# Optimization experiments

Hardware: AMD Instinct MI355X
Metric: run time of the kernel (lower is better)

## Reference

```python
import jax, jax.numpy as jnp
import numpy as np

N, M, E, HID, H = 50000, 4000, 320000, 128, 2
EPS = 1e-5  # torch BatchNorm1d eps


def _lrelu(x):
    return jnp.where(x >= 0, x, 0.2 * x)


def _bn(x, g, b):
    # BatchNorm1d in training mode: biased batch statistics over dim 0
    m = x.mean(0)
    v = ((x - m) ** 2).mean(0)
    return g * (x - m) * jax.lax.rsqrt(v + EPS) + b


def _seg_softmax(a, idx, n):
    # softmax of a[E,heads] normalized per node index idx (PyG softmax)
    mx = jax.ops.segment_max(a, idx, num_segments=n)
    e = jnp.exp(a - mx[idx])
    s = jax.ops.segment_sum(e, idx, num_segments=n)
    return e / s[idx]


def _hgconv(x, he_n, he_e, he_w, W, att, bias, heads):
    # PyG HypergraphConv(use_attention=True, concat=False)
    xl = (x @ W).reshape(N, heads, HID)                  # lin(x) -> [N,heads,C]
    # hyperedge_attr = incidence^T @ x  (matches to_dense_adj path in HGAT)
    ea = jax.ops.segment_sum(x[he_n], he_e, num_segments=M)  # [M,F]
    eal = (ea @ W).reshape(M, heads, HID)                # lin(hyperedge_attr)
    a = (jnp.concatenate([xl[he_n], eal[he_e]], axis=-1) * att[0]).sum(-1)  # [E,heads]
    a = _seg_softmax(_lrelu(a), he_n, N)
    # degree normalizations
    Dn = jax.ops.segment_sum(he_w[he_e], he_n, num_segments=N)
    Dinv = jnp.where(Dn > 0, 1.0 / Dn, 0.0)
    Bn = jax.ops.segment_sum(jnp.ones((E,), x.dtype), he_e, num_segments=M)
    Binv = jnp.where(Bn > 0, 1.0 / Bn, 0.0)
    # node -> hyperedge
    m1 = Binv[he_e][:, None, None] * xl[he_n] * a[..., None]
    eo = jax.ops.segment_sum(m1, he_e, num_segments=M)   # [M,heads,C]
    # hyperedge -> node
    m2 = Dinv[he_n][:, None, None] * eo[he_e] * a[..., None]
    out = jax.ops.segment_sum(m2, he_n, num_segments=N)  # [N,heads,C]
    return out.mean(1) + bias                            # concat=False -> head mean


def _forward(x, he_w, lin1_w, lin1_b, bn1_g, bn1_b, h1_w, h1_att, h1_b,
             bn2_g, bn2_b, h2_w, h2_att, h2_b, bn3_g, bn3_b,
             lin2_w, lin2_b, bn4_g, bn4_b, he_n, he_e):
    src = x
    x = _bn(_lrelu(x @ lin1_w + lin1_b), bn1_g, bn1_b)
    x2 = _hgconv(x, he_n, he_e, he_w, h1_w, h1_att, h1_b, H)
    x = _bn(x + x2, bn2_g, bn2_b)
    x2 = _hgconv(x, he_n, he_e, he_w, h2_w, h2_att, h2_b, 1)
    x = _bn(x + x2, bn3_g, bn3_b)
    x = _lrelu(x @ lin2_w + lin2_b)
    return _bn(src + x, bn4_g, bn4_b)


def setup_inputs() -> dict:
    key = jax.random.key(0)
    ks = jax.random.split(key, 10)
    s = 0.05
    he_n = jax.random.randint(ks[0], (E,), 0, N, dtype=jnp.int32)
    he_e = (jnp.arange(E, dtype=jnp.int32) % M)  # every hyperedge id used
    return {
        'x': jax.random.normal(ks[1], (N, 128), jnp.float32),
        'he_n': he_n, 'he_e': he_e,
        'he_w': jnp.ones((M,), jnp.float32),
        'lin1_w': jax.random.normal(ks[2], (128, HID), jnp.float32) * s,
        'lin1_b': jnp.zeros((HID,), jnp.float32),
        'bn1_g': jnp.ones((HID,), jnp.float32), 'bn1_b': jnp.zeros((HID,), jnp.float32),
        'h1_w': jax.random.normal(ks[3], (HID, H * HID), jnp.float32) * s,
        'h1_att': jax.random.normal(ks[4], (1, H, 2 * HID), jnp.float32) * s,
        'h1_b': jnp.zeros((HID,), jnp.float32),
        'bn2_g': jnp.ones((HID,), jnp.float32), 'bn2_b': jnp.zeros((HID,), jnp.float32),
        'h2_w': jax.random.normal(ks[5], (HID, HID), jnp.float32) * s,
        'h2_att': jax.random.normal(ks[6], (1, 1, 2 * HID), jnp.float32) * s,
        'h2_b': jnp.zeros((HID,), jnp.float32),
        'bn3_g': jnp.ones((HID,), jnp.float32), 'bn3_b': jnp.zeros((HID,), jnp.float32),
        'lin2_w': jax.random.normal(ks[7], (HID, 128), jnp.float32) * s,
        'lin2_b': jnp.zeros((128,), jnp.float32),
        'bn4_g': jnp.ones((128,), jnp.float32), 'bn4_b': jnp.zeros((128,), jnp.float32),
    }


def reference(x, he_n, he_e, he_w, lin1_w, lin1_b, bn1_g, bn1_b, h1_w, h1_att, h1_b,
              bn2_g, bn2_b, h2_w, h2_att, h2_b, bn3_g, bn3_b,
              lin2_w, lin2_b, bn4_g, bn4_b):
    return _forward(x, he_w, lin1_w, lin1_b, bn1_g, bn1_b, h1_w, h1_att, h1_b,
                    bn2_g, bn2_b, h2_w, h2_att, h2_b, bn3_g, bn3_b,
                    lin2_w, lin2_b, bn4_g, bn4_b, he_n, he_e)
```

## Files before the change

kernel.cpp:

```cpp
#include <hip/hip_runtime.h>
#include <math.h>

constexpr int Nn = 50000;
constexpr int Mm = 4000;
constexpr int Ee = 320000;
constexpr int KPB = Ee / Mm;
constexpr float BINV = 1.0f / (float)KPB;
constexpr float EPSf = 1e-5f;
constexpr int NBKT = 16;
constexpr int NBSCAN = 49;

__device__ __forceinline__ float lrelu_f(float x) { return x >= 0.f ? x : 0.2f * x; }

__device__ __forceinline__ float wave_sum(float v) {
#pragma unroll
    for (int o = 32; o >= 1; o >>= 1) v += __shfl_xor(v, o, 64);
    return v;
}

__device__ __forceinline__ void finalize_to_lds(const float* __restrict__ st,
                                                const float* __restrict__ g,
                                                const float* __restrict__ b,
                                                float* ABsh, int t) {
    if (t < 128) {
        double ds = 0, dq = 0;
#pragma unroll
        for (int i = 0; i < NBKT; i++) {
            ds += (double)st[i * 256 + t];
            dq += (double)st[i * 256 + 128 + t];
        }
        double mean = ds / (double)Nn;
        double var = dq / (double)Nn - mean * mean;
        float rstd = (float)(1.0 / sqrt(var + (double)EPSf));
        float A = g[t] * rstd;
        ABsh[t] = A;
        ABsh[128 + t] = b[t] - (float)mean * A;
    }
    __syncthreads();
}

__device__ void scan_body(const int* __restrict__ counts, int* __restrict__ offs,
                          int b, int t) {
    __shared__ int sdi[256];
    int pre = 0;
    for (int i = t; i < b * 1024; i += 256) pre += counts[i];
    sdi[t] = pre;
    __syncthreads();
    for (int st = 128; st >= 1; st >>= 1) {
        if (t < st) sdi[t] += sdi[t + st];
        __syncthreads();
    }
    int run0 = sdi[0];
    __syncthreads();
    int c4[4];
    int s = 0;
#pragma unroll
    for (int i = 0; i < 4; i++) {
        int n = b * 1024 + t * 4 + i;
        c4[i] = (n < Nn) ? counts[n] : 0;
        s += c4[i];
    }
    sdi[t] = s;
    __syncthreads();
    for (int off = 1; off < 256; off <<= 1) {
        int v = (t >= off) ? sdi[t - off] : 0;
        __syncthreads();
        sdi[t] += v;
        __syncthreads();
    }
    int run = sdi[t] - s + run0;
#pragma unroll
    for (int i = 0; i < 4; i++) {
        int n = b * 1024 + t * 4 + i;
        if (n < Nn) offs[n] = run;
        run += c4[i];
    }
    if (b == NBSCAN - 1 && t == 255) offs[Nn] = run0 + sdi[255];
}

template <int ROWS, bool LRELU, bool PROBN, bool RESID, bool STATS, bool PACKH2, bool SCANX>
__global__ __launch_bounds__(256) void gemmT(const float* __restrict__ A, size_t aystride,
                                             const float* __restrict__ B, int ldb,
                                             const float* __restrict__ bias, float scale,
                                             const float* __restrict__ stIn,
                                             const float* __restrict__ fing,
                                             const float* __restrict__ finb,
                                             const float* __restrict__ resid,
                                             float* __restrict__ stF,
                                             float* __restrict__ C, int ldc, int R,
                                             int gemmBlocksX,
                                             const int* __restrict__ counts,
                                             int* __restrict__ offs) {
    constexpr int RPT = ROWS / 16;
    const int t = threadIdx.x;
    if (SCANX && (int)blockIdx.x >= gemmBlocksX) {
        if (blockIdx.y == 0) scan_body(counts, offs, blockIdx.x - gemmBlocksX, t);
        return;
    }
    __shared__ float As[16][ROWS + 4];
    __shared__ float Bs[16][128];
    __shared__ float Sred[STATS ? 16 : 1][STATS ? 128 : 1];
    __shared__ float ABsh[PROBN ? 256 : 1];
    const int ty = t >> 4, tx = t & 15;
    const int row0 = blockIdx.x * ROWS;
    const int bcol = blockIdx.y * 128;
    A += (size_t)blockIdx.y * aystride;

    if (PROBN) finalize_to_lds(stIn, fing, finb, ABsh, t);

    float4 acc[RPT][2];
#pragma unroll
    for (int i = 0; i < RPT; i++)
#pragma unroll
        for (int q = 0; q < 2; q++) acc[i][q] = make_float4(0.f, 0.f, 0.f, 0.f);

    for (int k0 = 0; k0 < 128; k0 += 16) {
        if (ROWS == 64) {
            int r = t >> 2, kc = (t & 3) * 4;
            int rr = row0 + r;
            rr = rr < R ? rr : R - 1;
            float4 av = *(const float4*)(A + (size_t)rr * 128 + k0 + kc);
            if (PROBN) {
                float4 sA = *(const float4*)&ABsh[k0 + kc];
                float4 sB = *(const float4*)&ABsh[128 + k0 + kc];
                av.x = av.x * sA.x + sB.x; av.y = av.y * sA.y + sB.y;
                av.z = av.z * sA.z + sB.z; av.w = av.w * sA.w + sB.w;
            }
            As[kc + 0][r] = av.x; As[kc + 1][r] = av.y;
            As[kc + 2][r] = av.z; As[kc + 3][r] = av.w;
        } else {
            int r = t >> 3, kc = (t & 7) * 2;
            int rr = row0 + r;
            rr = rr < R ? rr : R - 1;
            float2 av = *(const float2*)(A + (size_t)rr * 128 + k0 + kc);
            if (PROBN) {
                av.x = av.x * ABsh[k0 + kc] + ABsh[128 + k0 + kc];
                av.y = av.y * ABsh[k0 + kc + 1] + ABsh[128 + k0 + kc + 1];
            }
            As[kc + 0][r] = av.x;
            As[kc + 1][r] = av.y;
        }
        {
            int kk = t >> 5, c4 = (t & 31) * 4;
            float4 bv0 = *(const float4*)(B + (size_t)(k0 + kk) * ldb + bcol + c4);
            float4 bv1 = *(const float4*)(B + (size_t)(k0 + kk + 8) * ldb + bcol + c4);
            *(float4*)&Bs[kk][c4] = bv0;
            *(float4*)&Bs[kk + 8][c4] = bv1;
        }
        __syncthreads();
#pragma unroll
        for (int kk = 0; kk < 16; kk++) {
            float ar[RPT];
            if (RPT == 4) {
                float4 a4 = *(const float4*)&As[kk][ty * 4];
                ar[0] = a4.x; ar[1] = a4.y; ar[2] = a4.z; ar[3] = a4.w;
            } else {
                float2 a2 = *(const float2*)&As[kk][ty * 2];
                ar[0] = a2.x; ar[RPT - 1] = a2.y;
            }
            float4 b0 = *(const float4*)&Bs[kk][4 * tx];
            float4 b1 = *(const float4*)&Bs[kk][64 + 4 * tx];
#pragma unroll
            for (int i = 0; i < RPT; i++) {
                acc[i][0].x = fmaf(ar[i], b0.x, acc[i][0].x);
                acc[i][0].y = fmaf(ar[i], b0.y, acc[i][0].y);
                acc[i][0].z = fmaf(ar[i], b0.z, acc[i][0].z);
                acc[i][0].w = fmaf(ar[i], b0.w, acc[i][0].w);
                acc[i][1].x = fmaf(ar[i], b1.x, acc[i][1].x);
                acc[i][1].y = fmaf(ar[i], b1.y, acc[i][1].y);
                acc[i][1].z = fmaf(ar[i], b1.z, acc[i][1].z);
                acc[i][1].w = fmaf(ar[i], b1.w, acc[i][1].w);
            }
        }
        __syncthreads();
    }

    float4 bv0 = make_float4(0.f, 0.f, 0.f, 0.f), bv1 = bv0;
    if (bias) {
        bv0 = *(const float4*)(bias + bcol + 4 * tx);
        bv1 = *(const float4*)(bias + bcol + 64 + 4 * tx);
    }
    float4 cs0 = make_float4(0.f, 0.f, 0.f, 0.f), cs1 = cs0, cq0 = cs0, cq1 = cs0;
#pragma unroll
    for (int i = 0; i < RPT; i++) {
        int row = row0 + ty * RPT + i;
        if (row >= R) continue;
        float4 v0, v1;
        v0.x = acc[i][0].x * scale + bv0.x; v0.y = acc[i][0].y * scale + bv0.y;
        v0.z = acc[i][0].z * scale + bv0.z; v0.w = acc[i][0].w * scale + bv0.w;
        v1.x = acc[i][1].x * scale + bv1.x; v1.y = acc[i][1].y * scale + bv1.y;
        v1.z = acc[i][1].z * scale + bv1.z; v1.w = acc[i][1].w * scale + bv1.w;
        if (LRELU) {
            v0.x = lrelu_f(v0.x); v0.y = lrelu_f(v0.y); v0.z = lrelu_f(v0.z); v0.w = lrelu_f(v0.w);
            v1.x = lrelu_f(v1.x); v1.y = lrelu_f(v1.y); v1.z = lrelu_f(v1.z); v1.w = lrelu_f(v1.w);
        }
        if (RESID) {
            float4 r0 = *(const float4*)(resid + (size_t)row * 128 + bcol + 4 * tx);
            float4 r1 = *(const float4*)(resid + (size_t)row * 128 + bcol + 64 + 4 * tx);
            v0.x += r0.x; v0.y += r0.y; v0.z += r0.z; v0.w += r0.w;
            v1.x += r1.x; v1.y += r1.y; v1.z += r1.z; v1.w += r1.w;
        }
        if (PACKH2) {
            int h = blockIdx.y;
            float* c0 = C + (size_t)row * ldc + 8 * tx + 2 * h;
            *(float2*)(c0) = make_float2(v0.x, v0.y);
            *(float2*)(c0 + 4) = make_float2(v0.z, v0.w);
            float* c1 = C + (size_t)row * ldc + 128 + 8 * tx + 2 * h;
            *(float2*)(c1) = make_float2(v1.x, v1.y);
            *(float2*)(c1 + 4) = make_float2(v1.z, v1.w);
        } else {
            *(float4*)(C + (size_t)row * ldc + bcol + 4 * tx) = v0;
            *(float4*)(C + (size_t)row * ldc + bcol + 64 + 4 * tx) = v1;
        }
        if (STATS) {
            cs0.x += v0.x; cs0.y += v0.y; cs0.z += v0.z; cs0.w += v0.w;
            cs1.x += v1.x; cs1.y += v1.y; cs1.z += v1.z; cs1.w += v1.w;
            cq0.x += v0.x * v0.x; cq0.y += v0.y * v0.y; cq0.z += v0.z * v0.z; cq0.w += v0.w * v0.w;
            cq1.x += v1.x * v1.x; cq1.y += v1.y * v1.y; cq1.z += v1.z * v1.z; cq1.w += v1.w * v1.w;
        }
    }
    if (STATS) {
        int bkt = blockIdx.x & (NBKT - 1);
#pragma unroll
        for (int pass = 0; pass < 2; pass++) {
            *(float4*)&Sred[ty][4 * tx] = pass ? cq0 : cs0;
            *(float4*)&Sred[ty][64 + 4 * tx] = pass ? cq1 : cs1;
            __syncthreads();
            if (t < 128) {
                float tot = 0.f;
#pragma unroll
                for (int r = 0; r < 16; r++) tot += Sred[r][t];
                atomicAdd(&stF[bkt * 256 + pass * 128 + t], tot);
            }
            __syncthreads();
        }
    }
}

__global__ void count_edges_watt(const int* __restrict__ he_n, int* __restrict__ counts,
                                 const float* __restrict__ h1_w, const float* __restrict__ h1_att,
                                 const float* __restrict__ h2_w, const float* __restrict__ h2_att,
                                 float* __restrict__ wnA, float* __restrict__ weA) {
    int t = threadIdx.x;
    if (blockIdx.x == 1250) {
        for (int j = 0; j < 3; j++) {
            int id = t + 256 * j;
            if (id >= 768) break;
            int which = id / 384;
            int rem = id % 384;
            int h3 = rem >> 7, k = rem & 127;
            float s = 0.f;
            if (h3 < 2) {
                const float* wrow = h1_w + (size_t)k * 256 + h3 * 128;
                const float* arow = h1_att + h3 * 256 + which * 128;
                for (int c = 0; c < 128; c++) s += wrow[c] * arow[c];
            } else {
                const float* wrow = h2_w + (size_t)k * 128;
                const float* arow = h2_att + which * 128;
                for (int c = 0; c < 128; c++) s += wrow[c] * arow[c];
            }
            (which ? weA : wnA)[h3 * 128 + k] = s;
        }
        return;
    }
    int e = blockIdx.x * 256 + t;
    if (e < Ee) atomicAdd(&counts[he_n[e]], 1);
}

template <int H, bool FILL>
__global__ __launch_bounds__(256) void bn_dots(const float* __restrict__ X,
                                               const float* __restrict__ stIn,
                                               const float* __restrict__ fing,
                                               const float* __restrict__ finb,
                                               float* __restrict__ ABout,
                                               const float* __restrict__ wn,
                                               const float* __restrict__ we,
                                               float* __restrict__ an,
                                               float* __restrict__ pe,
                                               const int* __restrict__ he_n,
                                               const int* __restrict__ offs,
                                               int* __restrict__ cursor,
                                               int* __restrict__ eid, int mainBlocks) {
    int t = threadIdx.x;
    if (FILL && (int)blockIdx.x >= mainBlocks) {
        int e = (blockIdx.x - mainBlocks) * 256 + t;
        if (e < Ee) {
            int n = he_n[e];
            int p = atomicAdd(&cursor[n], 1);
            eid[offs[n] + p] = e;
        }
        return;
    }
    __shared__ float ABsh[256];
    finalize_to_lds(stIn, fing, finb, ABsh, t);
    if (blockIdx.x == 0) ABout[t] = ABsh[t];
    int w = t >> 6, lane = t & 63;
    float a0 = ABsh[lane], a1 = ABsh[lane + 64];
    float b0 = ABsh[128 + lane], b1 = ABsh[192 + lane];
    float wn0[H], wn1[H], we0[H], we1[H];
#pragma unroll
    for (int h = 0; h < H; h++) {
        wn0[h] = wn[h * 128 + lane]; wn1[h] = wn[h * 128 + 64 + lane];
        we0[h] = we[h * 128 + lane]; we1[h] = we[h * 128 + 64 + lane];
    }
#pragma unroll
    for (int nn = 0; nn < 4; nn++) {
        int row = blockIdx.x * 16 + w * 4 + nn;
        const float* xr = X + (size_t)row * 128;
        float v0 = xr[lane] * a0 + b0;
        float v1 = xr[lane + 64] * a1 + b1;
        float pv[H], qv[H];
#pragma unroll
        for (int h = 0; h < H; h++) {
            pv[h] = wave_sum(v0 * wn0[h] + v1 * wn1[h]);
            qv[h] = wave_sum(v0 * we0[h] + v1 * we1[h]);
        }
        if (lane == 0) {
            if (H == 2) {
                *(float2*)&an[row * 2] = make_float2(pv[0], pv[1]);
                *(float2*)&pe[row * 2] = make_float2(qv[0], qv[1]);
            } else {
                an[row] = pv[0];
                pe[row] = qv[0];
            }
        }
    }
}

__global__ __launch_bounds__(256) void bn_out(const float* __restrict__ X,
                                              const float* __restrict__ stIn,
                                              const float* __restrict__ fing,
                                              const float* __restrict__ finb,
                                              float* __restrict__ Y) {
    __shared__ float ABsh[256];
    int t = threadIdx.x;
    finalize_to_lds(stIn, fing, finb, ABsh, t);
    int w = t >> 6, lane = t & 63;
    float a0 = ABsh[lane], a1 = ABsh[lane + 64];
    float b0 = ABsh[128 + lane], b1 = ABsh[192 + lane];
#pragma unroll
    for (int nn = 0; nn < 4; nn++) {
        int row = blockIdx.x * 16 + w * 4 + nn;
        const float* xr = X + (size_t)row * 128;
        float* yr = Y + (size_t)row * 128;
        yr[lane] = xr[lane] * a0 + b0;
        yr[lane + 64] = xr[lane + 64] * a1 + b1;
    }
}

template <int H>
__global__ __launch_bounds__(256) void ea_from_pe(const int* __restrict__ he_n,
                                                  const float* __restrict__ pe,
                                                  float* __restrict__ ae) {
    int w = threadIdx.x >> 6, lane = threadIdx.x & 63;
    int m = blockIdx.x * 4 + w;
    if (m >= Mm) return;
    float s[H];
#pragma unroll
    for (int h = 0; h < H; h++) s[h] = 0.f;
    for (int k = lane; k < KPB; k += 64) {
        int idx = he_n[m + k * Mm];
        if (H == 2) {
            float2 p2 = *(const float2*)(pe + (size_t)idx * 2);
            s[0] += p2.x;
            s[H - 1] += p2.y;
        } else {
            s[0] += pe[idx];
        }
    }
#pragma unroll
    for (int h = 0; h < H; h++) s[h] = wave_sum(s[h]);
    if (lane == 0)
#pragma unroll
        for (int h = 0; h < H; h++) ae[m * H + h] = s[h];
}

template <int H>
__global__ __launch_bounds__(256) void seg_softmax(const int* __restrict__ offs,
                                                   const int* __restrict__ eid,
                                                   const float* __restrict__ an,
                                                   const float* __restrict__ ae,
                                                   const float* __restrict__ he_w,
                                                   float* __restrict__ aw,
                                                   float* __restrict__ sdl) {
    int t = threadIdx.x;
    int wv = t >> 6, lane = t & 63;
    int q = lane >> 3, li = lane & 7;
    int n = blockIdx.x * 32 + wv * 8 + q;
    bool valid = n < Nn;
    int base = valid ? offs[n] : 0;
    int deg = valid ? offs[n + 1] - base : 0;
    float anv[H];
#pragma unroll
    for (int h = 0; h < H; h++) anv[h] = valid ? an[n * H + h] : 0.f;

    bool h0 = li < deg, h1 = li + 8 < deg;
    int e0 = 0, e1 = 0, m0 = 0, m1 = 0;
    float l0[H], l1[H];
    float mx[H];
#pragma unroll
    for (int h = 0; h < H; h++) { mx[h] = -INFINITY; l0[h] = 0.f; l1[h] = 0.f; }
    if (h0) {
        e0 = eid[base + li];
        m0 = e0 % Mm;
#pragma unroll
        for (int h = 0; h < H; h++) {
            l0[h] = lrelu_f(anv[h] + ae[m0 * H + h]);
            mx[h] = fmaxf(mx[h], l0[h]);
        }
    }
    if (h1) {
        e1 = eid[base + li + 8];
        m1 = e1 % Mm;
#pragma unroll
        for (int h = 0; h < H; h++) {
            l1[h] = lrelu_f(anv[h] + ae[m1 * H + h]);
            mx[h] = fmaxf(mx[h], l1[h]);
        }
    }
    for (int c = li + 16; c < deg; c += 8) {
        int e = eid[base + c];
        int m = e % Mm;
#pragma unroll
        for (int h = 0; h < H; h++) mx[h] = fmaxf(mx[h], lrelu_f(anv[h] + ae[m * H + h]));
    }
#pragma unroll
    for (int h = 0; h < H; h++) {
#pragma unroll
        for (int o = 1; o <= 4; o <<= 1) mx[h] = fmaxf(mx[h], __shfl_xor(mx[h], o, 64));
    }
    float sm[H], p0[H], p1[H];
#pragma unroll
    for (int h = 0; h < H; h++) { sm[h] = 0.f; p0[h] = 0.f; p1[h] = 0.f; }
    float dn = 0.f;
    if (h0) {
        dn += he_w[m0];
#pragma unroll
        for (int h = 0; h < H; h++) { p0[h] = expf(l0[h] - mx[h]); sm[h] += p0[h]; }
    }
    if (h1) {
        dn += he_w[m1];
#pragma unroll
        for (int h = 0; h < H; h++) { p1[h] = expf(l1[h] - mx[h]); sm[h] += p1[h]; }
    }
    for (int c = li + 16; c < deg; c += 8) {
        int e = eid[base + c];
        int m = e % Mm;
        dn += he_w[m];
#pragma unroll
        for (int h = 0; h < H; h++) sm[h] += expf(lrelu_f(anv[h] + ae[m * H + h]) - mx[h]);
    }
#pragma unroll
    for (int o = 1; o <= 4; o <<= 1) dn += __shfl_xor(dn, o, 64);
#pragma unroll
    for (int h = 0; h < H; h++) {
#pragma unroll
        for (int o = 1; o <= 4; o <<= 1) sm[h] += __shfl_xor(sm[h], o, 64);
    }
    float Dv = dn > 0.f ? 1.0f / dn : 0.0f;
    float premul = Dv * (H == 2 ? 0.5f : 1.0f);
    if (h0) {
        float p[H];
#pragma unroll
        for (int h = 0; h < H; h++) p[h] = p0[h] / sm[h];
        if (H == 2) {
            *(float2*)(aw + (size_t)e0 * 2) = make_float2(p[0], p[1]);
            *(float4*)(sdl + (size_t)(base + li) * 4) =
                make_float4(__int_as_float(m0), p[0] * premul, p[H - 1] * premul, 0.f);
        } else {
            aw[e0] = p[0];
            *(float2*)(sdl + (size_t)(base + li) * 2) = make_float2(__int_as_float(m0), p[0] * premul);
        }
    }
    if (h1) {
        float p[H];
#pragma unroll
        for (int h = 0; h < H; h++) p[h] = p1[h] / sm[h];
        if (H == 2) {
            *(float2*)(aw + (size_t)e1 * 2) = make_float2(p[0], p[1]);
            *(float4*)(sdl + (size_t)(base + li + 8) * 4) =
                make_float4(__int_as_float(m1), p[0] * premul, p[H - 1] * premul, 0.f);
        } else {
            aw[e1] = p[0];
            *(float2*)(sdl + (size_t)(base + li + 8) * 2) =
                make_float2(__int_as_float(m1), p[0] * premul);
        }
    }
    for (int c = li + 16; c < deg; c += 8) {
        int e = eid[base + c];
        int m = e % Mm;
        float p[H];
#pragma unroll
        for (int h = 0; h < H; h++) p[h] = expf(lrelu_f(anv[h] + ae[m * H + h]) - mx[h]) / sm[h];
        if (H == 2) {
            *(float2*)(aw + (size_t)e * 2) = make_float2(p[0], p[1]);
            *(float4*)(sdl + (size_t)(base + c) * 4) =
                make_float4(__int_as_float(m), p[0] * premul, p[H - 1] * premul, 0.f);
        } else {
            aw[e] = p[0];
            *(float2*)(sdl + (size_t)(base + c) * 2) = make_float2(__int_as_float(m), p[0] * premul);
        }
    }
}

template <int H>
__global__ __launch_bounds__(256) void s_build(const float* __restrict__ X,
                                               const float* __restrict__ AB,
                                               const int* __restrict__ he_n,
                                               const float* __restrict__ aw,
                                               float* __restrict__ S) {
    __shared__ int idx[KPB];
    __shared__ float av[KPB][H];
    __shared__ float red[8][H][128];
    int m = blockIdx.x, t = threadIdx.x;
    int g = t >> 5, l = t & 31;
    if (t < KPB) idx[t] = he_n[m + t * Mm];
    for (int q2 = t; q2 < KPB * H; q2 += 256) {
        int k = q2 / H, h = q2 - k * H;
        av[k][h] = aw[(size_t)(m + k * Mm) * H + h];
    }
    __syncthreads();
    float4 A4 = ((const float4*)AB)[l];
    float4 B4 = ((const float4*)(AB + 128))[l];
    float4 acc[H];
#pragma unroll
    for (int h = 0; h < H; h++) acc[h] = make_float4(0.f, 0.f, 0.f, 0.f);
#pragma unroll
    for (int kk = 0; kk < KPB / 8; kk++) {
        int k = g + kk * 8;
        float4 v = ((const float4*)(X + (size_t)idx[k] * 128))[l];
        v.x = v.x * A4.x + B4.x;
        v.y = v.y * A4.y + B4.y;
        v.z = v.z * A4.z + B4.z;
        v.w = v.w * A4.w + B4.w;
#pragma unroll
        for (int h = 0; h < H; h++) {
            float a = av[k][h];
            acc[h].x = fmaf(a, v.x, acc[h].x);
            acc[h].y = fmaf(a, v.y, acc[h].y);
            acc[h].z = fmaf(a, v.z, acc[h].z);
            acc[h].w = fmaf(a, v.w, acc[h].w);
        }
    }
#pragma unroll
    for (int h = 0; h < H; h++) *(float4*)&red[g][h][l * 4] = acc[h];
    __syncthreads();
    if (t < 32 * H) {
        int h = t >> 5, l2 = t & 31;
        float4 s = make_float4(0.f, 0.f, 0.f, 0.f);
#pragma unroll
        for (int gg = 0; gg < 8; gg++) {
            float4 r = *(const float4*)&red[gg][h][l2 * 4];
            s.x += r.x; s.y += r.y; s.z += r.z; s.w += r.w;
        }
        ((float4*)(S + ((size_t)h * Mm + m) * 128))[l2] = s;
    }
}

template <int H>
__global__ __launch_bounds__(256) void node_agg(const int* __restrict__ offs,
                                                const float* __restrict__ sdl,
                                                const float* __restrict__ eo,
                                                const float* __restrict__ bias,
                                                const float* __restrict__ AB,
                                                float* __restrict__ stF,
                                                float* __restrict__ T) {
    __shared__ float smem[4][256];
    __shared__ float redS[4][128], redQ[4][128];
    int t = threadIdx.x;
    int w = t >> 6, lane = t & 63;
    int n0 = blockIdx.x * 16 + w * 4;
    int o = offs[n0 + (lane < 4 ? lane : 4)];
    int b0 = __shfl(o, 0, 64);
    int b1 = __shfl(o, 1, 64);
    int b2 = __shfl(o, 2, 64);
    int b3 = __shfl(o, 3, 64);
    int b4 = __shfl(o, 4, 64);
    int cnt = b4 - b0;
    int cnt64 = cnt < 64 ? cnt : 64;

    if (lane < cnt64) {
        int slot = b0 + lane;
        if (H == 2) {
            *(float4*)&smem[w][4 * lane] = *(const float4*)(sdl + (size_t)slot * 4);
        } else {
            *(float2*)&smem[w][2 * lane] = *(const float2*)(sdl + (size_t)slot * 2);
        }
    }
    __syncthreads();

    int s1 = min(b1 - b0, cnt64), s2 = min(b2 - b0, cnt64), s3 = min(b3 - b0, cnt64);
    float2 acc0 = make_float2(0.f, 0.f), acc1 = acc0, acc2 = acc0, acc3 = acc0;

#define NA_BODY(ACC, CBEG, CEND)                                                \
    {                                                                           \
        int c = (CBEG);                                                         \
        for (; c + 1 < (CEND); c += 2) {                                        \
            if (H == 2) {                                                       \
                float4 sa = *(const float4*)&smem[w][4 * c];                    \
                float4 sb = *(const float4*)&smem[w][4 * (c + 1)];              \
                float4 ea = *(const float4*)(eo + (size_t)__float_as_int(sa.x) * 256 + 4 * lane); \
                float4 eb = *(const float4*)(eo + (size_t)__float_as_int(sb.x) * 256 + 4 * lane); \
                ACC.x += sa.y * ea.x + sa.z * ea.z + sb.y * eb.x + sb.z * eb.z; \
                ACC.y += sa.y * ea.y + sa.z * ea.w + sb.y * eb.y + sb.z * eb.w; \
            } else {                                                            \
                float2 sa = *(const float2*)&smem[w][2 * c];                    \
                float2 sb = *(const float2*)&smem[w][2 * (c + 1)];              \
                float2 ea = *(const float2*)(eo + (size_t)__float_as_int(sa.x) * 128 + 2 * lane); \
                float2 eb = *(const float2*)(eo + (size_t)__float_as_int(sb.x) * 128 + 2 * lane); \
                ACC.x += sa.y * ea.x + sb.y * eb.x;                             \
                ACC.y += sa.y * ea.y + sb.y * eb.y;                             \
            }                                                                   \
        }                                                                       \
        if (c < (CEND)) {                                                       \
            if (H == 2) {                                                       \
                float4 sa = *(const float4*)&smem[w][4 * c];                    \
                float4 ea = *(const float4*)(eo + (size_t)__float_as_int(sa.x) * 256 + 4 * lane); \
                ACC.x += sa.y * ea.x + sa.z * ea.z;                             \
                ACC.y += sa.y * ea.y + sa.z * ea.w;                             \
            } else {                                                            \
                float2 sa = *(const float2*)&smem[w][2 * c];                    \
                float2 ea = *(const float2*)(eo + (size_t)__float_as_int(sa.x) * 128 + 2 * lane); \
                ACC.x += sa.y * ea.x;                                           \
                ACC.y += sa.y * ea.y;                                           \
            }                                                                   \
        }                                                                       \
    }
    NA_BODY(acc0, 0, s1)
    NA_BODY(acc1, s1, s2)
    NA_BODY(acc2, s2, s3)
    NA_BODY(acc3, s3, cnt64)
#undef NA_BODY

    for (int ss = 64; ss < cnt; ss++) {
        int slot = b0 + ss;
        int j = (slot >= b1) + (slot >= b2) + (slot >= b3);
        float cx, cy;
        if (H == 2) {
            float4 v = *(const float4*)(sdl + (size_t)slot * 4);
            float4 ev = *(const float4*)(eo + (size_t)__float_as_int(v.x) * 256 + 4 * lane);
            cx = v.y * ev.x + v.z * ev.z;
            cy = v.y * ev.y + v.z * ev.w;
        } else {
            float2 v = *(const float2*)(sdl + (size_t)slot * 2);
            float2 ev = *(const float2*)(eo + (size_t)__float_as_int(v.x) * 128 + 2 * lane);
            cx = v.y * ev.x;
            cy = v.y * ev.y;
        }
        if (j == 0) { acc0.x += cx; acc0.y += cy; }
        else if (j == 1) { acc1.x += cx; acc1.y += cy; }
        else if (j == 2) { acc2.x += cx; acc2.y += cy; }
        else { acc3.x += cx; acc3.y += cy; }
    }

    int col = 2 * lane;
    float2 A2 = *(const float2*)(AB + col);
    float2 B2 = *(const float2*)(AB + 128 + col);
    float2 bi = *(const float2*)(bias + col);
    float cs0 = 0.f, cs1 = 0.f, cq0 = 0.f, cq1 = 0.f;
    float2 accs[4] = {acc0, acc1, acc2, acc3};
#pragma unroll
    for (int j = 0; j < 4; j++) {
        int n = n0 + j;
        float2 xr = *(const float2*)(T + (size_t)n * 128 + col);
        float r0 = xr.x * A2.x + B2.x + bi.x + accs[j].x;
        float r1 = xr.y * A2.y + B2.y + bi.y + accs[j].y;
        *(float2*)(T + (size_t)n * 128 + col) = make_float2(r0, r1);
        cs0 += r0; cs1 += r1;
        cq0 += r0 * r0; cq1 += r1 * r1;
    }
    redS[w][col] = cs0; redS[w][col + 1] = cs1;
    redQ[w][col] = cq0; redQ[w][col + 1] = cq1;
    __syncthreads();
    if (t < 128) {
        float s = 0.f, qq = 0.f;
#pragma unroll
        for (int ww = 0; ww < 4; ww++) { s += redS[ww][t]; qq += redQ[ww][t]; }
        int bkt = blockIdx.x & (NBKT - 1);
        atomicAdd(&stF[bkt * 256 + t], s);
        atomicAdd(&stF[bkt * 256 + 128 + t], qq);
    }
}

extern "C" void kernel_launch(void* const* d_in, const int* in_sizes, int n_in,
                              void* d_out, int out_size, void* d_ws, size_t ws_size,
                              hipStream_t stream) {
    const float* x = (const float*)d_in[0];
    const int* he_n = (const int*)d_in[1];
    const float* he_w = (const float*)d_in[3];
    const float* lin1_w = (const float*)d_in[4];
    const float* lin1_b = (const float*)d_in[5];
    const float* bn1_g = (const float*)d_in[6];
    const float* bn1_b = (const float*)d_in[7];
    const float* h1_w = (const float*)d_in[8];
    const float* h1_att = (const float*)d_in[9];
    const float* h1_b = (const float*)d_in[10];
    const float* bn2_g = (const float*)d_in[11];
    const float* bn2_b = (const float*)d_in[12];
    const float* h2_w = (const float*)d_in[13];
    const float* h2_att = (const float*)d_in[14];
    const float* h2_b = (const float*)d_in[15];
    const float* bn3_g = (const float*)d_in[16];
    const float* bn3_b = (const float*)d_in[17];
    const float* lin2_w = (const float*)d_in[18];
    const float* lin2_b = (const float*)d_in[19];
    const float* bn4_g = (const float*)d_in[20];
    const float* bn4_b = (const float*)d_in[21];
    float* out = (float*)d_out;

    char* ws = (char*)d_ws;
    size_t off = 0;
    auto alloc = [&](size_t bytes) -> char* {
        char* p = ws + off;
        off = (off + bytes + 255) & ~(size_t)255;
        return p;
    };
    int* counts = (int*)alloc((size_t)Nn * 4);
    int* cursor = (int*)alloc((size_t)Nn * 4);
    float* stats = (float*)alloc((size_t)4 * NBKT * 256 * 4);
    size_t zbytes = off;
    int* offs = (int*)alloc((size_t)(Nn + 1) * 4);
    int* eid = (int*)alloc((size_t)Ee * 4);
    float* an = (float*)alloc((size_t)Nn * 2 * 4);
    float* pe = (float*)alloc((size_t)Nn * 2 * 4);
    float* ae = (float*)alloc((size_t)Mm * 2 * 4);
    float* aw = (float*)alloc((size_t)Ee * 2 * 4);
    float* sdl = (float*)alloc((size_t)Ee * 4 * 4);
    float* S = (float*)alloc((size_t)2 * Mm * 128 * 4);
    float* eo = (float*)alloc((size_t)2 * Mm * 128 * 4);
    float* wnA = (float*)alloc(384 * 4);
    float* weA = (float*)alloc(384 * 4);
    float* AB = (float*)alloc(2 * 256 * 4);
    float* buf = (float*)alloc((size_t)Nn * 128 * 4);

    float* st0 = stats;
    float* st1 = stats + NBKT * 256;
    float* st2 = stats + 2 * NBKT * 256;
    float* st3 = stats + 3 * NBKT * 256;
    float *AB1 = AB, *AB2 = AB + 256;

    hipMemsetAsync(d_ws, 0, zbytes, stream);

    constexpr int GB32 = (Nn + 31) / 32;
    count_edges_watt<<<1251, 256, 0, stream>>>(he_n, counts, h1_w, h1_att, h2_w, h2_att,
                                               wnA, weA);

    gemmT<32, true, false, false, true, false, true><<<dim3(GB32 + NBSCAN, 1), 256, 0, stream>>>(
        x, 0, lin1_w, 128, lin1_b, 1.f, nullptr, nullptr, nullptr, nullptr, st0, buf, 128, Nn,
        GB32, counts, offs);
    bn_dots<2, true><<<3125 + 1250, 256, 0, stream>>>(buf, st0, bn1_g, bn1_b, AB1, wnA, weA,
                                                      an, pe, he_n, offs, cursor, eid, 3125);

    ea_from_pe<2><<<Mm / 4, 256, 0, stream>>>(he_n, pe, ae);
    seg_softmax<2><<<(Nn + 31) / 32, 256, 0, stream>>>(offs, eid, an, ae, he_w, aw, sdl);
    s_build<2><<<Mm, 256, 0, stream>>>(buf, AB1, he_n, aw, S);
    gemmT<32, false, false, false, false, true, false><<<dim3(125, 2), 256, 0, stream>>>(
        S, (size_t)Mm * 128, h1_w, 256, nullptr, BINV, nullptr, nullptr, nullptr, nullptr,
        nullptr, eo, 256, Mm, 125, nullptr, nullptr);
    node_agg<2><<<3125, 256, 0, stream>>>(offs, sdl, eo, h1_b, AB1, st1, buf);

    bn_dots<1, false><<<3125, 256, 0, stream>>>(buf, st1, bn2_g, bn2_b, AB2, wnA + 256,
                                                weA + 256, an, pe, nullptr, nullptr, nullptr,
                                                nullptr, 3125);

    ea_from_pe<1><<<Mm / 4, 256, 0, stream>>>(he_n, pe, ae);
    seg_softmax<1><<<(Nn + 31) / 32, 256, 0, stream>>>(offs, eid, an, ae, he_w, aw, sdl);
    s_build<1><<<Mm, 256, 0, stream>>>(buf, AB2, he_n, aw, S);
    gemmT<32, false, false, false, false, false, false><<<dim3(125, 1), 256, 0, stream>>>(
        S, 0, h2_w, 128, nullptr, BINV, nullptr, nullptr, nullptr, nullptr, nullptr,
        eo, 128, Mm, 125, nullptr, nullptr);
    node_agg<1><<<3125, 256, 0, stream>>>(offs, sdl, eo, h2_b, AB2, st2, buf);

    gemmT<32, true, true, true, true, false, false><<<dim3(GB32, 1), 256, 0, stream>>>(
        buf, 0, lin2_w, 128, lin2_b, 1.f, st2, bn3_g, bn3_b, x, st3, buf, 128, Nn,
        GB32, nullptr, nullptr);
    bn_out<<<3125, 256, 0, stream>>>(buf, st3, bn4_g, bn4_b, out);
}
```

Baseline: 400.7 us.

## Fuse hyperedge GEMM into s_build and scatter layer-2 edge attention via atomics

s_build now processes four hyperedges per block, keeps the aggregated S rows in LDS and multiplies them by the conv weight directly, writing eo. This removes the S intermediate buffer and the separate gemmT launches. For layer 2, bn_dots atomically scatters each node's edge-projection dot into a zeroed per-hyperedge array, replacing the ea_from_pe kernel. The trade-offs are a weight GEMM with strided global weight reads and low parallelism (1000 blocks), plus atomic contention on only 4000 targets.

```diff
diff --git a/kernel.cpp b/kernel.cpp
--- a/kernel.cpp
+++ b/kernel.cpp
@@ -9,6 +9,7 @@
 constexpr float EPSf = 1e-5f;
 constexpr int NBKT = 16;
 constexpr int NBSCAN = 49;
+constexpr int MB = 4;
 
 __device__ __forceinline__ float lrelu_f(float x) { return x >= 0.f ? x : 0.2f * x; }
 
@@ -78,8 +79,8 @@
     if (b == NBSCAN - 1 && t == 255) offs[Nn] = run0 + sdi[255];
 }
 
-template <int ROWS, bool LRELU, bool PROBN, bool RESID, bool STATS, bool PACKH2, bool SCANX>
-__global__ __launch_bounds__(256) void gemmT(const float* __restrict__ A, size_t aystride,
+template <int ROWS, bool LRELU, bool PROBN, bool RESID, bool STATS, bool SCANX>
+__global__ __launch_bounds__(256) void gemmT(const float* __restrict__ A,
                                              const float* __restrict__ B, int ldb,
                                              const float* __restrict__ bias, float scale,
                                              const float* __restrict__ stIn,
@@ -94,7 +95,7 @@
     constexpr int RPT = ROWS / 16;
     const int t = threadIdx.x;
     if (SCANX && (int)blockIdx.x >= gemmBlocksX) {
-        if (blockIdx.y == 0) scan_body(counts, offs, blockIdx.x - gemmBlocksX, t);
+        scan_body(counts, offs, blockIdx.x - gemmBlocksX, t);
         return;
     }
     __shared__ float As[16][ROWS + 4];
@@ -103,8 +104,6 @@
     __shared__ float ABsh[PROBN ? 256 : 1];
     const int ty = t >> 4, tx = t & 15;
     const int row0 = blockIdx.x * ROWS;
-    const int bcol = blockIdx.y * 128;
-    A += (size_t)blockIdx.y * aystride;
 
     if (PROBN) finalize_to_lds(stIn, fing, finb, ABsh, t);
 
@@ -115,20 +114,7 @@
         for (int q = 0; q < 2; q++) acc[i][q] = make_float4(0.f, 0.f, 0.f, 0.f);
 
     for (int k0 = 0; k0 < 128; k0 += 16) {
-        if (ROWS == 64) {
-            int r = t >> 2, kc = (t & 3) * 4;
-            int rr = row0 + r;
-            rr = rr < R ? rr : R - 1;
-            float4 av = *(const float4*)(A + (size_t)rr * 128 + k0 + kc);
-            if (PROBN) {
-                float4 sA = *(const float4*)&ABsh[k0 + kc];
-                float4 sB = *(const float4*)&ABsh[128 + k0 + kc];
-                av.x = av.x * sA.x + sB.x; av.y = av.y * sA.y + sB.y;
-                av.z = av.z * sA.z + sB.z; av.w = av.w * sA.w + sB.w;
-            }
-            As[kc + 0][r] = av.x; As[kc + 1][r] = av.y;
-            As[kc + 2][r] = av.z; As[kc + 3][r] = av.w;
-        } else {
+        {
             int r = t >> 3, kc = (t & 7) * 2;
             int rr = row0 + r;
             rr = rr < R ? rr : R - 1;
@@ -142,8 +128,8 @@
         }
         {
             int kk = t >> 5, c4 = (t & 31) * 4;
-            float4 bv0 = *(const float4*)(B + (size_t)(k0 + kk) * ldb + bcol + c4);
-            float4 bv1 = *(const float4*)(B + (size_t)(k0 + kk + 8) * ldb + bcol + c4);
+            float4 bv0 = *(const float4*)(B + (size_t)(k0 + kk) * ldb + c4);
+            float4 bv1 = *(const float4*)(B + (size_t)(k0 + kk + 8) * ldb + c4);
             *(float4*)&Bs[kk][c4] = bv0;
             *(float4*)&Bs[kk + 8][c4] = bv1;
         }
@@ -151,13 +137,8 @@
 #pragma unroll
         for (int kk = 0; kk < 16; kk++) {
             float ar[RPT];
-            if (RPT == 4) {
-                float4 a4 = *(const float4*)&As[kk][ty * 4];
-                ar[0] = a4.x; ar[1] = a4.y; ar[2] = a4.z; ar[3] = a4.w;
-            } else {
-                float2 a2 = *(const float2*)&As[kk][ty * 2];
-                ar[0] = a2.x; ar[RPT - 1] = a2.y;
-            }
+            float2 a2 = *(const float2*)&As[kk][ty * 2];
+            ar[0] = a2.x; ar[RPT - 1] = a2.y;
             float4 b0 = *(const float4*)&Bs[kk][4 * tx];
             float4 b1 = *(const float4*)&Bs[kk][64 + 4 * tx];
 #pragma unroll
@@ -177,8 +158,8 @@
 
     float4 bv0 = make_float4(0.f, 0.f, 0.f, 0.f), bv1 = bv0;
     if (bias) {
-        bv0 = *(const float4*)(bias + bcol + 4 * tx);
-        bv1 = *(const float4*)(bias + bcol + 64 + 4 * tx);
+        bv0 = *(const float4*)(bias + 4 * tx);
+        bv1 = *(const float4*)(bias + 64 + 4 * tx);
     }
     float4 cs0 = make_float4(0.f, 0.f, 0.f, 0.f), cs1 = cs0, cq0 = cs0, cq1 = cs0;
 #pragma unroll
@@ -195,23 +176,13 @@
             v1.x = lrelu_f(v1.x); v1.y = lrelu_f(v1.y); v1.z = lrelu_f(v1.z); v1.w = lrelu_f(v1.w);
         }
         if (RESID) {
-            float4 r0 = *(const float4*)(resid + (size_t)row * 128 + bcol + 4 * tx);
-            float4 r1 = *(const float4*)(resid + (size_t)row * 128 + bcol + 64 + 4 * tx);
+            float4 r0 = *(const float4*)(resid + (size_t)row * 128 + 4 * tx);
+            float4 r1 = *(const float4*)(resid + (size_t)row * 128 + 64 + 4 * tx);
             v0.x += r0.x; v0.y += r0.y; v0.z += r0.z; v0.w += r0.w;
             v1.x += r1.x; v1.y += r1.y; v1.z += r1.z; v1.w += r1.w;
         }
-        if (PACKH2) {
-            int h = blockIdx.y;
-            float* c0 = C + (size_t)row * ldc + 8 * tx + 2 * h;
-            *(float2*)(c0) = make_float2(v0.x, v0.y);
-            *(float2*)(c0 + 4) = make_float2(v0.z, v0.w);
-            float* c1 = C + (size_t)row * ldc + 128 + 8 * tx + 2 * h;
-            *(float2*)(c1) = make_float2(v1.x, v1.y);
-            *(float2*)(c1 + 4) = make_float2(v1.z, v1.w);
-        } else {
-            *(float4*)(C + (size_t)row * ldc + bcol + 4 * tx) = v0;
-            *(float4*)(C + (size_t)row * ldc + bcol + 64 + 4 * tx) = v1;
-        }
+        *(float4*)(C + (size_t)row * ldc + 4 * tx) = v0;
+        *(float4*)(C + (size_t)row * ldc + 64 + 4 * tx) = v1;
         if (STATS) {
             cs0.x += v0.x; cs0.y += v0.y; cs0.z += v0.z; cs0.w += v0.w;
             cs1.x += v1.x; cs1.y += v1.y; cs1.z += v1.z; cs1.w += v1.w;
@@ -267,7 +238,7 @@
     if (e < Ee) atomicAdd(&counts[he_n[e]], 1);
 }
 
-template <int H, bool FILL>
+template <int H, bool FILL, bool SCATTER>
 __global__ __launch_bounds__(256) void bn_dots(const float* __restrict__ X,
                                                const float* __restrict__ stIn,
                                                const float* __restrict__ fing,
@@ -280,7 +251,8 @@
                                                const int* __restrict__ he_n,
                                                const int* __restrict__ offs,
                                                int* __restrict__ cursor,
-                                               int* __restrict__ eid, int mainBlocks) {
+                                               int* __restrict__ eid, int mainBlocks,
+                                               float* __restrict__ aeOut) {
     int t = threadIdx.x;
     if (FILL && (int)blockIdx.x >= mainBlocks) {
         int e = (blockIdx.x - mainBlocks) * 256 + t;
@@ -321,7 +293,15 @@
                 *(float2*)&pe[row * 2] = make_float2(qv[0], qv[1]);
             } else {
                 an[row] = pv[0];
-                pe[row] = qv[0];
+                if (!SCATTER) pe[row] = qv[0];
+            }
+        }
+        if (SCATTER) {
+            int base = offs[row];
+            int deg = offs[row + 1] - base;
+            for (int c = lane; c < deg; c += 64) {
+                int e = eid[base + c];
+                atomicAdd(&aeOut[e % Mm], qv[0]);
             }
         }
     }
@@ -508,52 +488,114 @@
                                                const float* __restrict__ AB,
                                                const int* __restrict__ he_n,
                                                const float* __restrict__ aw,
-                                               float* __restrict__ S) {
-    __shared__ int idx[KPB];
-    __shared__ float av[KPB][H];
+                                               const float* __restrict__ W, int ldw,
+                                               float* __restrict__ eo) {
+    __shared__ int idx[MB][KPB];
+    __shared__ float av[MB][KPB][H];
     __shared__ float red[8][H][128];
-    int m = blockIdx.x, t = threadIdx.x;
+    __shared__ float S_lds[MB][H][128];
+    __shared__ float eo_lds[MB][H * 128];
+    int m0 = blockIdx.x * MB, t = threadIdx.x;
     int g = t >> 5, l = t & 31;
-    if (t < KPB) idx[t] = he_n[m + t * Mm];
-    for (int q2 = t; q2 < KPB * H; q2 += 256) {
-        int k = q2 / H, h = q2 - k * H;
-        av[k][h] = aw[(size_t)(m + k * Mm) * H + h];
+    for (int q = t; q < MB * KPB; q += 256) {
+        int k = q >> 2, mi = q & (MB - 1);
+        idx[mi][k] = he_n[m0 + mi + k * Mm];
+    }
+    for (int q = t; q < MB * KPB * H; q += 256) {
+        int mi = q & (MB - 1);
+        int rest = q >> 2;
+        int k = rest / H, h = rest - k * H;
+        av[mi][k][h] = aw[(size_t)(m0 + mi + k * Mm) * H + h];
     }
     __syncthreads();
     float4 A4 = ((const float4*)AB)[l];
     float4 B4 = ((const float4*)(AB + 128))[l];
-    float4 acc[H];
-#pragma unroll
-    for (int h = 0; h < H; h++) acc[h] = make_float4(0.f, 0.f, 0.f, 0.f);
-#pragma unroll
-    for (int kk = 0; kk < KPB / 8; kk++) {
-        int k = g + kk * 8;
-        float4 v = ((const float4*)(X + (size_t)idx[k] * 128))[l];
-        v.x = v.x * A4.x + B4.x;
-        v.y = v.y * A4.y + B4.y;
-        v.z = v.z * A4.z + B4.z;
-        v.w = v.w * A4.w + B4.w;
-#pragma unroll
-        for (int h = 0; h < H; h++) {
-            float a = av[k][h];
-            acc[h].x = fmaf(a, v.x, acc[h].x);
-            acc[h].y = fmaf(a, v.y, acc[h].y);
-            acc[h].z = fmaf(a, v.z, acc[h].z);
-            acc[h].w = fmaf(a, v.w, acc[h].w);
-        }
-    }
-#pragma unroll
-    for (int h = 0; h < H; h++) *(float4*)&red[g][h][l * 4] = acc[h];
+#pragma unroll
+    for (int mi = 0; mi < MB; mi++) {
+        float4 acc[H];
+#pragma unroll
+        for (int h = 0; h < H; h++) acc[h] = make_float4(0.f, 0.f, 0.f, 0.f);
+#pragma unroll
+        for (int kk = 0; kk < KPB / 8; kk++) {
+            int k = g + kk * 8;
+            float4 v = ((const float4*)(X + (size_t)idx[mi][k] * 128))[l];
+            v.x = v.x * A4.x + B4.x;
+            v.y = v.y * A4.y + B4.y;
+            v.z = v.z * A4.z + B4.z;
+            v.w = v.w * A4.w + B4.w;
+#pragma unroll
+            for (int h = 0; h < H; h++) {
+                float a = av[mi][k][h];
+                acc[h].x = fmaf(a, v.x, acc[h].x);
+                acc[h].y = fmaf(a, v.y, acc[h].y);
+                acc[h].z = fmaf(a, v.z, acc[h].z);
+                acc[h].w = fmaf(a, v.w, acc[h].w);
+            }
+        }
+#pragma unroll
+        for (int h = 0; h < H; h++) *(float4*)&red[g][h][l * 4] = acc[h];
+        __syncthreads();
+        if (t < 32 * H) {
+            int h = t >> 5, l2 = t & 31;
+            float4 s = make_float4(0.f, 0.f, 0.f, 0.f);
+#pragma unroll
+            for (int gg = 0; gg < 8; gg++) {
+                float4 r = *(const float4*)&red[gg][h][l2 * 4];
+                s.x += r.x; s.y += r.y; s.z += r.z; s.w += r.w;
+            }
+            *(float4*)&S_lds[mi][h][l2 * 4] = s;
+        }
+        __syncthreads();
+    }
+
+    if (H == 2) {
+        int h = t >> 7, c = t & 127;
+        float a0 = 0.f, a1 = 0.f, a2 = 0.f, a3 = 0.f;
+        const float* wp = W + h * 128 + c;
+#pragma unroll 4
+        for (int k = 0; k < 128; k++) {
+            float wv = wp[(size_t)k * ldw];
+            a0 = fmaf(S_lds[0][h][k], wv, a0);
+            a1 = fmaf(S_lds[1][h][k], wv, a1);
+            a2 = fmaf(S_lds[2][h][k], wv, a2);
+            a3 = fmaf(S_lds[3][h][k], wv, a3);
+        }
+        int pos = 4 * (c >> 1) + 2 * h + (c & 1);
+        eo_lds[0][pos] = a0 * BINV;
+        eo_lds[1][pos] = a1 * BINV;
+        eo_lds[2][pos] = a2 * BINV;
+        eo_lds[3][pos] = a3 * BINV;
+    } else {
+        int c = t & 127, half = t >> 7;
+        float a0 = 0.f, a1 = 0.f, a2 = 0.f, a3 = 0.f;
+        const float* wp = W + c;
+#pragma unroll 4
+        for (int k = half * 64; k < half * 64 + 64; k++) {
+            float wv = wp[(size_t)k * ldw];
+            a0 = fmaf(S_lds[0][0][k], wv, a0);
+            a1 = fmaf(S_lds[1][0][k], wv, a1);
+            a2 = fmaf(S_lds[2][0][k], wv, a2);
+            a3 = fmaf(S_lds[3][0][k], wv, a3);
+        }
+        float* part = &red[0][0][0];
+        part[(half * 4 + 0) * 128 + c] = a0;
+        part[(half * 4 + 1) * 128 + c] = a1;
+        part[(half * 4 + 2) * 128 + c] = a2;
+        part[(half * 4 + 3) * 128 + c] = a3;
+        __syncthreads();
+        if (t < 128) {
+#pragma unroll
+            for (int mi = 0; mi < MB; mi++)
+                eo_lds[mi][t] = (part[(0 * 4 + mi) * 128 + t] + part[(4 + mi) * 128 + t]) * BINV;
+        }
+    }
     __syncthreads();
-    if (t < 32 * H) {
-        int h = t >> 5, l2 = t & 31;
-        float4 s = make_float4(0.f, 0.f, 0.f, 0.f);
-#pragma unroll
-        for (int gg = 0; gg < 8; gg++) {
-            float4 r = *(const float4*)&red[gg][h][l2 * 4];
-            s.x += r.x; s.y += r.y; s.z += r.z; s.w += r.w;
-        }
-        ((float4*)(S + ((size_t)h * Mm + m) * 128))[l2] = s;
+    int total4 = MB * H * 32;
+    if (t < total4) {
+        int per = H * 32;
+        int mi = t / per, off = t % per;
+        *(float4*)(eo + (size_t)(m0 + mi) * (H * 128) + off * 4) =
+            *(const float4*)&eo_lds[mi][off * 4];
     }
 }
 
@@ -718,6 +760,7 @@
     int* counts = (int*)alloc((size_t)Nn * 4);
     int* cursor = (int*)alloc((size_t)Nn * 4);
     float* stats = (float*)alloc((size_t)4 * NBKT * 256 * 4);
+    float* ae2 = (float*)alloc((size_t)Mm * 4);
     size_t zbytes = off;
     int* offs = (int*)alloc((size_t)(Nn + 1) * 4);
     int* eid = (int*)alloc((size_t)Ee * 4);
@@ -726,7 +769,6 @@
     float* ae = (float*)alloc((size_t)Mm * 2 * 4);
     float* aw = (float*)alloc((size_t)Ee * 2 * 4);
     float* sdl = (float*)alloc((size_t)Ee * 4 * 4);
-    float* S = (float*)alloc((size_t)2 * Mm * 128 * 4);
     float* eo = (float*)alloc((size_t)2 * Mm * 128 * 4);
     float* wnA = (float*)alloc(384 * 4);
     float* weA = (float*)alloc(384 * 4);
@@ -745,34 +787,27 @@
     count_edges_watt<<<1251, 256, 0, stream>>>(he_n, counts, h1_w, h1_att, h2_w, h2_att,
                                                wnA, weA);
 
-    gemmT<32, true, false, false, true, false, true><<<dim3(GB32 + NBSCAN, 1), 256, 0, stream>>>(
-        x, 0, lin1_w, 128, lin1_b, 1.f, nullptr, nullptr, nullptr, nullptr, st0, buf, 128, Nn,
+    gemmT<32, true, false, false, true, true><<<GB32 + NBSCAN, 256, 0, stream>>>(
+        x, lin1_w, 128, lin1_b, 1.f, nullptr, nullptr, nullptr, nullptr, st0, buf, 128, Nn,
         GB32, counts, offs);
-    bn_dots<2, true><<<3125 + 1250, 256, 0, stream>>>(buf, st0, bn1_g, bn1_b, AB1, wnA, weA,
-                                                      an, pe, he_n, offs, cursor, eid, 3125);
+    bn_dots<2, true, false><<<3125 + 1250, 256, 0, stream>>>(
+        buf, st0, bn1_g, bn1_b, AB1, wnA, weA, an, pe, he_n, offs, cursor, eid, 3125, nullptr);
 
     ea_from_pe<2><<<Mm / 4, 256, 0, stream>>>(he_n, pe, ae);
     seg_softmax<2><<<(Nn + 31) / 32, 256, 0, stream>>>(offs, eid, an, ae, he_w, aw, sdl);
-    s_build<2><<<Mm, 256, 0, stream>>>(buf, AB1, he_n, aw, S);
-    gemmT<32, false, false, false, false, true, false><<<dim3(125, 2), 256, 0, stream>>>(
-        S, (size_t)Mm * 128, h1_w, 256, nullptr, BINV, nullptr, nullptr, nullptr, nullptr,
-        nullptr, eo, 256, Mm, 125, nullptr, nullptr);
+    s_build<2><<<Mm / MB, 256, 0, stream>>>(buf, AB1, he_n, aw, h1_w, 256, eo);
     node_agg<2><<<3125, 256, 0, stream>>>(offs, sdl, eo, h1_b, AB1, st1, buf);
 
-    bn_dots<1, false><<<3125, 256, 0, stream>>>(buf, st1, bn2_g, bn2_b, AB2, wnA + 256,
-                                                weA + 256, an, pe, nullptr, nullptr, nullptr,
-                                                nullptr, 3125);
-
-    ea_from_pe<1><<<Mm / 4, 256, 0, stream>>>(he_n, pe, ae);
-    seg_softmax<1><<<(Nn + 31) / 32, 256, 0, stream>>>(offs, eid, an, ae, he_w, aw, sdl);
-    s_build<1><<<Mm, 256, 0, stream>>>(buf, AB2, he_n, aw, S);
-    gemmT<32, false, false, false, false, false, false><<<dim3(125, 1), 256, 0, stream>>>(
-        S, 0, h2_w, 128, nullptr, BINV, nullptr, nullptr, nullptr, nullptr, nullptr,
-        eo, 128, Mm, 125, nullptr, nullptr);
+    bn_dots<1, false, true><<<3125, 256, 0, stream>>>(
+        buf, st1, bn2_g, bn2_b, AB2, wnA + 256, weA + 256, an, pe, nullptr, offs, nullptr,
+        eid, 3125, ae2);
+
+    seg_softmax<1><<<(Nn + 31) / 32, 256, 0, stream>>>(offs, eid, an, ae2, he_w, aw, sdl);
+    s_build<1><<<Mm / MB, 256, 0, stream>>>(buf, AB2, he_n, aw, h2_w, 128, eo);
     node_agg<1><<<3125, 256, 0, stream>>>(offs, sdl, eo, h2_b, AB2, st2, buf);
 
-    gemmT<32, true, true, true, true, false, false><<<dim3(GB32, 1), 256, 0, stream>>>(
-        buf, 0, lin2_w, 128, lin2_b, 1.f, st2, bn3_g, bn3_b, x, st3, buf, 128, Nn,
+    gemmT<32, true, true, true, true, false><<<GB32, 256, 0, stream>>>(
+        buf, lin2_w, 128, lin2_b, 1.f, st2, bn3_g, bn3_b, x, st3, buf, 128, Nn,
         GB32, nullptr, nullptr);
     bn_out<<<3125, 256, 0, stream>>>(buf, st3, bn4_g, bn4_b, out);
 }
```

Result: no change. 404.0 us (+0.8%).
